# Optimization experiments

Measured on AMD Instinct MI355X. Metric: run time of the kernel, lower is better.

The kernel has to match this reference:

```python
import jax, jax.numpy as jnp
import numpy as np

B, S, HID = 1, 4096, 2048
NH, D = 16, 128
RATIO, TOPK, WIN = 4, 8, 128
ROPE_DIM = D // 2  # partial RoPE on first half of head_dim
EPS = 1e-6
NEG = -1e30


def rmsnorm(x, w):
    return x * jax.lax.rsqrt(jnp.mean(x * x, axis=-1, keepdims=True) + EPS) * w


def apply_rope(x, pos):
    # x: [..., L, D_head]; pos: [L] integer positions
    half = ROPE_DIM // 2
    inv = 1.0 / (10000.0 ** (jnp.arange(half, dtype=x.dtype) * (2.0 / ROPE_DIM)))
    ang = pos.astype(x.dtype)[:, None] * inv[None, :]  # [L, half]
    cos, sin = jnp.cos(ang), jnp.sin(ang)
    x1, x2, rest = x[..., :half], x[..., half:ROPE_DIM], x[..., ROPE_DIM:]
    return jnp.concatenate([x1 * cos - x2 * sin, x1 * sin + x2 * cos, rest], axis=-1)


def setup_inputs() -> dict:
    key = jax.random.key(0)
    ks = jax.random.split(key, 16)
    n = jax.random.normal
    s = 0.02
    return {
        "hidden_states": n(ks[0], (B, S, HID), jnp.float32),
        "Wq": n(ks[1], (HID, NH * D)) * s, "bq": jnp.zeros((NH * D,)),
        "Wcmp": n(ks[2], (HID, 1)) * s, "bcmp": jnp.zeros((1,)),
        "Wk": n(ks[3], (HID, D)) * s, "bk": jnp.zeros((D,)),
        "Wv": n(ks[4], (HID, D)) * s, "bv": jnp.zeros((D,)),
        "Wlk": n(ks[5], (HID, NH * D)) * s, "blk": jnp.zeros((NH * D,)),
        "Wlv": n(ks[6], (HID, NH * D)) * s, "blv": jnp.zeros((NH * D,)),
        "qn_w": jnp.ones((D,)), "kn_w": jnp.ones((D,)),
        "Wo": n(ks[7], (NH * D, HID)) * s, "bo": jnp.zeros((HID,)),
    }


def reference(hidden_states, Wq, bq, Wcmp, bcmp, Wk, bk, Wv, bv, Wlk, blk, Wlv, blv, qn_w, kn_w, Wo, bo):
    Bq, Sq, _ = hidden_states.shape
    C = Sq // RATIO
    scale = 1.0 / jnp.sqrt(jnp.float32(D))
    pos = jnp.arange(Sq)

    q = (hidden_states @ Wq + bq).reshape(Bq, Sq, NH, D).transpose(0, 2, 1, 3)  # [B,H,S,D]
    q = apply_rope(rmsnorm(q, qn_w), pos)

    # learned KV compression: softmax-weighted pooling within each block of size RATIO
    w_log = (hidden_states @ Wcmp + bcmp).reshape(Bq, C, RATIO)
    w_cmp = jax.nn.softmax(w_log, axis=-1)
    entries = jnp.einsum('bcr,bcrh->bch', w_cmp, hidden_states.reshape(Bq, C, RATIO, HID))
    block_ends = jnp.arange(1, C + 1) * RATIO - 1  # [C] last position of each block

    ck = apply_rope(rmsnorm(entries @ Wk + bk, kn_w), block_ends)  # [B,C,D] shared kv head
    cv = entries @ Wv + bv  # [B,C,D]

    # top-k block-sparse attention over compressed entries (causal on block_ends)
    sc = jnp.einsum('bhsd,bcd->bhsc', q, ck) * scale  # [B,H,S,C]
    causal = block_ends[None, None, None, :] <= pos[None, None, :, None]
    sc = jnp.where(causal, sc, NEG)
    tv, ti = jax.lax.top_k(sc, TOPK)  # [B,H,S,K]
    sel = (tv > NEG / 2).astype(sc.dtype)
    m = jnp.max(tv, axis=-1, keepdims=True)
    e = jnp.exp(tv - m) * sel
    pw = e / jnp.maximum(e.sum(axis=-1, keepdims=True), 1e-9)
    v_g = cv[jnp.arange(Bq)[:, None, None, None], ti]  # [B,H,S,K,D] irregular gather
    ctx_sparse = jnp.einsum('bhsk,bhskd->bhsd', pw, v_g)

    lk = apply_rope(rmsnorm((hidden_states @ Wlk + blk).reshape(Bq, Sq, NH, D).transpose(0, 2, 1, 3), kn_w), pos)
    lv = (hidden_states @ Wlv + blv).reshape(Bq, Sq, NH, D).transpose(0, 2, 1, 3)
    nc = Sq // WIN
    qc = q.reshape(Bq, NH, nc, WIN, D)

    def windowize(x):
        prev = jnp.pad(x, ((0, 0), (0, 0), (WIN, 0), (0, 0)))[:, :, :-WIN].reshape(Bq, NH, nc, WIN, D)
        cur = x.reshape(Bq, NH, nc, WIN, D)
        return jnp.concatenate([prev, cur], axis=3)  # [B,H,nc,2W,D]

    kw, vw = windowize(lk), windowize(lv)
    i = jnp.arange(WIN)[:, None]
    j = jnp.arange(2 * WIN)[None, :]
    rel = i + WIN - j  # qpos - kpos within the chunk pair
    band = (rel >= 0) & (rel <= WIN)
    kpos_ok = (jnp.arange(nc)[:, None, None] * WIN - WIN + j[None]) >= 0  # zero-pad chunk invalid
    mask = band[None] & kpos_ok  # [nc,W,2W]
    sl = jnp.einsum('bhcqd,bhckd->bhcqk', qc, kw) * scale
    sl = jnp.where(mask[None, None], sl, NEG)
    pl = jax.nn.softmax(sl, axis=-1)
    ctx_local = jnp.einsum('bhcqk,bhckd->bhcqd', pl, vw).reshape(Bq, NH, Sq, D)

    merged = (ctx_sparse + ctx_local) * 0.5  # mean over the two branches
    out = merged.transpose(0, 2, 1, 3).reshape(Bq, Sq, NH * D) @ Wo + bo
    return out
```

## Files before the change

kernel.cpp:

```cpp
#include <hip/hip_runtime.h>
#include <hip/hip_bf16.h>
#include <hip/hip_fp16.h>
#include <stdint.h>

typedef __hip_bfloat16 bf16;
using bf16x8 = __attribute__((ext_vector_type(8))) short;
using half8  = __attribute__((ext_vector_type(8))) _Float16;
using f32x4  = __attribute__((ext_vector_type(4))) float;

#define S_LEN   4096
#define HID_    2048
#define NH_     16
#define D_      128
#define C_      1024
#define SCALE_  0.08838834764831845f
#define DESC_   (1.0 / 1048576.0)

__device__ __forceinline__ float bflo(uint32_t u) {
  uint32_t x = (u & 0xffffu) << 16; float f; __builtin_memcpy(&f, &x, 4); return f;
}
__device__ __forceinline__ float bfhi(uint32_t u) {
  uint32_t x = u & 0xffff0000u; float f; __builtin_memcpy(&f, &x, 4); return f;
}
__device__ __forceinline__ void storeC(float* p, float v) { *p = v; }
__device__ __forceinline__ void storeC(bf16* p, float v)  { *p = __float2bfloat16(v); }
__device__ __forceinline__ void split2(float x, _Float16& h, _Float16& l) {
  h = (_Float16)x; l = (_Float16)(x - (float)h);
}
__device__ __forceinline__ short bf2s(bf16 b) { short s; __builtin_memcpy(&s, &b, 2); return s; }

__global__ __launch_bounds__(256) void cvt_k(const float* __restrict__ src, bf16* __restrict__ dst) {
  int i = (blockIdx.x * 256 + threadIdx.x) * 4;
  float4 v = *(const float4*)(src + i);
  bf16 o[4] = {__float2bfloat16(v.x), __float2bfloat16(v.y),
               __float2bfloat16(v.z), __float2bfloat16(v.w)};
  *(uint2*)(dst + i) = *(uint2*)o;
}

__global__ __launch_bounds__(256) void split_ck_k(const float* __restrict__ ckvF,
                                                  _Float16* __restrict__ oh, _Float16* __restrict__ ol) {
  int idx = blockIdx.x * 256 + threadIdx.x;
  int c = idx >> 7, k = idx & 127;
  float x = ckvF[(size_t)c * 256 + k] * 1024.0f;
  _Float16 h, l; split2(x, h, l);
  oh[idx] = h; ol[idx] = l;
}

__global__ __launch_bounds__(256) void transpose_k(const float* __restrict__ src,
                                                   bf16* __restrict__ dst, int R, int N) {
  __shared__ float tile[64][65];
  const int c0 = blockIdx.x * 64, r0 = blockIdx.y * 64;
  const int t = threadIdx.x, cc = t & 63, rb = t >> 6;
#pragma unroll
  for (int i = 0; i < 16; ++i) {
    int r = rb + i * 4;
    tile[r][cc] = src[(size_t)(r0 + r) * N + c0 + cc];
  }
  __syncthreads();
#pragma unroll
  for (int i = 0; i < 16; ++i) {
    int r = rb + i * 4;
    dst[(size_t)(c0 + r) * R + r0 + cc] = __float2bfloat16(tile[cc][r]);
  }
}

__global__ __launch_bounds__(256) void trans_f32s(const float* __restrict__ src,
                                                  float* __restrict__ dst, int R, int N) {
  __shared__ float tile[64][65];
  const int c0 = blockIdx.x * 64, r0 = blockIdx.y * 64;
  const int t = threadIdx.x, cc = t & 63, rb = t >> 6;
#pragma unroll
  for (int i = 0; i < 16; ++i) {
    int r = rb + i * 4;
    tile[r][cc] = src[(size_t)(r0 + r) * N + c0 + cc];
  }
  __syncthreads();
#pragma unroll
  for (int i = 0; i < 16; ++i) {
    int r = rb + i * 4;
    dst[(size_t)(c0 + r) * R + r0 + cc] = tile[cc][r] * 1024.0f;
  }
}

__global__ __launch_bounds__(256) void trans_v_k(const bf16* __restrict__ lklv, bf16* __restrict__ VT) {
  __shared__ ushort tile[64][65];
  const int s0 = blockIdx.x * 64, c0 = blockIdx.y * 64;
  const int t = threadIdx.x, cc = t & 63, rb = t >> 6;
  const ushort* src = (const ushort*)lklv;
#pragma unroll
  for (int i = 0; i < 16; ++i) {
    int r = rb + i * 4;
    tile[r][cc] = src[(size_t)(s0 + r) * 4096 + 2048 + c0 + cc];
  }
  __syncthreads();
  ushort* dst = (ushort*)VT;
#pragma unroll
  for (int i = 0; i < 16; ++i) {
    int r = rb + i * 4;
    dst[(size_t)(c0 + r) * 4096 + s0 + cc] = tile[cc][r];
  }
}

__global__ void build_bias(const float* bq, const float* blk, const float* blv,
                           const float* bk, const float* bv, const float* bo,
                           float* bQ, float* bLKLV, float* bKV, float* bO) {
  int i = blockIdx.x * 256 + threadIdx.x;
  if (i < 2048)       bQ[i] = bq[i];
  else if (i < 6144)  { int j = i - 2048; bLKLV[j] = (j < 2048) ? blk[j] : blv[j - 2048]; }
  else if (i < 6400)  { int j = i - 6144; bKV[j] = (j < 128) ? bk[j] : bv[j - 128]; }
  else if (i < 8448)  bO[i - 6400] = bo[i - 6400];
}

template <typename OutT>
__global__ __launch_bounds__(256) void gemm_bt(const bf16* __restrict__ A, const bf16* __restrict__ BT,
                                               const float* __restrict__ bias, OutT* __restrict__ Cmat,
                                               int M, int N, int K, int lda) {
  __shared__ bf16 As[128 * 32];
  __shared__ bf16 Bs[128 * 32];
  const int t = threadIdx.x;
  const int wave = t >> 6, lane = t & 63;
  const int wr = wave >> 1, wc = wave & 1;
  const int quad = lane >> 4, l15 = lane & 15;
  const int bx = blockIdx.x * 128, by = blockIdx.y * 128;
  const int srow = t >> 2, scol = (t & 3) * 8;
  f32x4 acc[4][4] = {};
  const bf16* a0 = A + (size_t)(by + srow) * lda + scol;
  const bf16* a1 = A + (size_t)(by + 64 + srow) * lda + scol;
  const bf16* b0 = BT + (size_t)(bx + srow) * K + scol;
  const bf16* b1 = BT + (size_t)(bx + 64 + srow) * K + scol;
  for (int k0 = 0; k0 < K; k0 += 32) {
    __builtin_amdgcn_global_load_lds((const __attribute__((address_space(1))) void*)(a0 + k0),
                                     (__attribute__((address_space(3))) void*)(As + t * 8), 16, 0, 0);
    __builtin_amdgcn_global_load_lds((const __attribute__((address_space(1))) void*)(a1 + k0),
                                     (__attribute__((address_space(3))) void*)(As + 2048 + t * 8), 16, 0, 0);
    __builtin_amdgcn_global_load_lds((const __attribute__((address_space(1))) void*)(b0 + k0),
                                     (__attribute__((address_space(3))) void*)(Bs + t * 8), 16, 0, 0);
    __builtin_amdgcn_global_load_lds((const __attribute__((address_space(1))) void*)(b1 + k0),
                                     (__attribute__((address_space(3))) void*)(Bs + 2048 + t * 8), 16, 0, 0);
    __syncthreads();
    bf16x8 aF[4], bF[4];
#pragma unroll
    for (int i = 0; i < 4; ++i)
      aF[i] = *(const bf16x8*)(As + (wr * 64 + i * 16 + l15) * 32 + quad * 8);
#pragma unroll
    for (int j = 0; j < 4; ++j)
      bF[j] = *(const bf16x8*)(Bs + (wc * 64 + j * 16 + l15) * 32 + quad * 8);
#pragma unroll
    for (int i = 0; i < 4; ++i)
#pragma unroll
      for (int j = 0; j < 4; ++j)
        acc[i][j] = __builtin_amdgcn_mfma_f32_16x16x32_bf16(aF[i], bF[j], acc[i][j], 0, 0, 0);
    __syncthreads();
  }
#pragma unroll
  for (int i = 0; i < 4; ++i)
#pragma unroll
    for (int j = 0; j < 4; ++j)
#pragma unroll
      for (int r = 0; r < 4; ++r) {
        int row = by + wr * 64 + i * 16 + quad * 4 + r;
        int col = bx + wc * 64 + j * 16 + l15;
        storeC(&Cmat[(size_t)row * N + col], acc[i][j][r] + bias[col]);
      }
}

__global__ __launch_bounds__(256) void gemm_prec4(const float* __restrict__ A, const float* __restrict__ BT,
                                                  const float* __restrict__ bias, float* __restrict__ Cmat,
                                                  int M, int N, int K, int lda) {
  __shared__ _Float16 Ah[128 * 32], Al[128 * 32], Bh[128 * 32], Bl[128 * 32];
  const int t = threadIdx.x;
  const int wave = t >> 6, lane = t & 63;
  const int wr = wave >> 1, wc = wave & 1;
  const int quad = lane >> 4, l15 = lane & 15;
  const int bx = blockIdx.x * 128, by = blockIdx.y * 128;
  double acc[4][4][4] = {};
  for (int k0 = 0; k0 < K; k0 += 32) {
#pragma unroll
    for (int it = 0; it < 4; ++it) {
      int sl = t + it * 256;
      int isB = sl >> 9, s2 = sl & 511, r = s2 >> 2, g = s2 & 3;
      const float* src = isB ? (BT + (size_t)(bx + r) * K + k0 + g * 8)
                             : (A  + (size_t)(by + r) * lda + k0 + g * 8);
      float4 u = ((const float4*)src)[0];
      float4 v = ((const float4*)src)[1];
      float xs[8] = {u.x, u.y, u.z, u.w, v.x, v.y, v.z, v.w};
      half8 hh, ll;
#pragma unroll
      for (int e = 0; e < 8; ++e) {
        float x = isB ? xs[e] : xs[e] * 1024.0f;
        _Float16 h, l; split2(x, h, l);
        hh[e] = h; ll[e] = l;
      }
      _Float16* dh = (isB ? Bh : Ah) + r * 32 + g * 8;
      _Float16* dl = (isB ? Bl : Al) + r * 32 + g * 8;
      *(half8*)dh = hh;
      *(half8*)dl = ll;
    }
    __syncthreads();
    half8 aFh[4], aFl[4], bFh[4], bFl[4];
#pragma unroll
    for (int i = 0; i < 4; ++i) {
      int ro = (wr * 64 + i * 16 + l15) * 32 + quad * 8;
      aFh[i] = *(const half8*)(Ah + ro);
      aFl[i] = *(const half8*)(Al + ro);
    }
#pragma unroll
    for (int j = 0; j < 4; ++j) {
      int ro = (wc * 64 + j * 16 + l15) * 32 + quad * 8;
      bFh[j] = *(const half8*)(Bh + ro);
      bFl[j] = *(const half8*)(Bl + ro);
    }
#pragma unroll
    for (int i = 0; i < 4; ++i)
#pragma unroll
      for (int j = 0; j < 4; ++j) {
        f32x4 tt = {0.f, 0.f, 0.f, 0.f};
        tt = __builtin_amdgcn_mfma_f32_16x16x32_f16(aFl[i], bFl[j], tt, 0, 0, 0);
        tt = __builtin_amdgcn_mfma_f32_16x16x32_f16(aFl[i], bFh[j], tt, 0, 0, 0);
        tt = __builtin_amdgcn_mfma_f32_16x16x32_f16(aFh[i], bFl[j], tt, 0, 0, 0);
        tt = __builtin_amdgcn_mfma_f32_16x16x32_f16(aFh[i], bFh[j], tt, 0, 0, 0);
#pragma unroll
        for (int r = 0; r < 4; ++r) acc[i][j][r] += (double)tt[r];
      }
    __syncthreads();
  }
#pragma unroll
  for (int i = 0; i < 4; ++i)
#pragma unroll
    for (int j = 0; j < 4; ++j)
#pragma unroll
      for (int r = 0; r < 4; ++r) {
        int row = by + wr * 64 + i * 16 + quad * 4 + r;
        int col = bx + wc * 64 + j * 16 + l15;
        Cmat[(size_t)row * N + col] = (float)(acc[i][j][r] * DESC_ + (double)bias[col]);
      }
}

__global__ __launch_bounds__(256) void normrope64(float* __restrict__ base, const float* __restrict__ w,
                                                  int nRows, int hPerS, int sStride,
                                                  int posMul, int posAdd) {
  int row = blockIdx.x * 4 + (threadIdx.x >> 6);
  int lane = threadIdx.x & 63;
  if (row >= nRows) return;
  int s = row / hPerS, h = row - s * hPerS;
  float* p = base + (size_t)s * sStride + h * 128;
  double x0 = (double)p[lane];
  double x1 = (double)p[lane + 64];
  double ss = x0 * x0 + x1 * x1;
#pragma unroll
  for (int m = 32; m; m >>= 1) ss += __shfl_xor(ss, m, 64);
  double rstd = 1.0 / sqrt(ss * (1.0 / 128.0) + 1e-6);
  double n0 = x0 * rstd * (double)w[lane];
  double n1 = x1 * rstd * (double)w[lane + 64];
  double other = __shfl_xor(n0, 32, 64);
  int fi = lane & 31;
  float invf = 1.0f / (float)pow(10000.0, (double)fi * (1.0 / 32.0));
  float angf = (float)(s * posMul + posAdd) * invf;
  double ang = (double)angf;
  double cs = cos(ang), sn = sin(ang);
  double r0 = (lane < 32) ? (n0 * cs - other * sn) : (other * sn + n0 * cs);
  p[lane] = (float)r0;
  p[lane + 64] = (float)n1;
}

__global__ __launch_bounds__(256) void normrope64_q(float* __restrict__ base, const float* __restrict__ w,
                                                    _Float16* __restrict__ qh, _Float16* __restrict__ ql) {
  __shared__ double csd[32], snd[32];
  const int s = blockIdx.x;
  const int t = threadIdx.x, wv = t >> 6, lane = t & 63;
  if (t < 32) {
    float invf = 1.0f / (float)pow(10000.0, (double)t * (1.0 / 32.0));
    float angf = (float)s * invf;
    double ang = (double)angf;
    csd[t] = cos(ang);
    snd[t] = sin(ang);
  }
  __syncthreads();
  const int fi = lane & 31;
  float* ps = base + (size_t)s * HID_;
  for (int h = wv; h < 16; h += 4) {
    float* p = ps + h * 128;
    double x0 = (double)p[lane];
    double x1 = (double)p[lane + 64];
    double ss = x0 * x0 + x1 * x1;
#pragma unroll
    for (int m = 32; m; m >>= 1) ss += __shfl_xor(ss, m, 64);
    double rstd = 1.0 / sqrt(ss * (1.0 / 128.0) + 1e-6);
    double n0 = x0 * rstd * (double)w[lane];
    double n1 = x1 * rstd * (double)w[lane + 64];
    double other = __shfl_xor(n0, 32, 64);
    double cs = csd[fi], sn = snd[fi];
    double r0 = (lane < 32) ? (n0 * cs - other * sn) : (other * sn + n0 * cs);
    float f0 = (float)r0, f1 = (float)n1;
    p[lane] = f0;
    p[lane + 64] = f1;
    _Float16 h0, l0, h1, l1;
    split2(f0 * 1024.0f, h0, l0);
    split2(f1 * 1024.0f, h1, l1);
    size_t off = (size_t)s * HID_ + h * 128;
    qh[off + lane] = h0;       ql[off + lane] = l0;
    qh[off + 64 + lane] = h1;  ql[off + 64 + lane] = l1;
  }
}

__global__ __launch_bounds__(256) void normrope_bf_l(bf16* __restrict__ base, const float* __restrict__ w) {
  __shared__ float csf[32], snf[32];
  const int s = blockIdx.x;
  const int t = threadIdx.x, wv = t >> 6, lane = t & 63;
  if (t < 32) {
    float invf = 1.0f / (float)pow(10000.0, (double)t * (1.0 / 32.0));
    float ang = (float)s * invf;
    csf[t] = cosf(ang);
    snf[t] = sinf(ang);
  }
  __syncthreads();
  const int fi = lane & 31;
  bf16* ps = base + (size_t)s * 4096;
  for (int h = wv; h < 16; h += 4) {
    bf16* p = ps + h * 128;
    float x0 = __bfloat162float(p[lane]);
    float x1 = __bfloat162float(p[lane + 64]);
    float ss = x0 * x0 + x1 * x1;
#pragma unroll
    for (int m = 32; m; m >>= 1) ss += __shfl_xor(ss, m, 64);
    float rstd = rsqrtf(ss * 0.0078125f + 1e-6f);
    float n0 = x0 * rstd * w[lane];
    float n1 = x1 * rstd * w[lane + 64];
    float other = __shfl_xor(n0, 32, 64);
    float cs = csf[fi], sn = snf[fi];
    float r0 = (lane < 32) ? (n0 * cs - other * sn) : (other * sn + n0 * cs);
    p[lane] = __float2bfloat16(r0);
    p[lane + 64] = __float2bfloat16(n1);
  }
}

__global__ __launch_bounds__(256) void wlog_k(const float* __restrict__ hidden, const float* __restrict__ wcmp,
                                              const float* __restrict__ bcmp, float* __restrict__ wlog) {
  int s = blockIdx.x * 4 + (threadIdx.x >> 6);
  int lane = threadIdx.x & 63;
  const float* hp = hidden + (size_t)s * HID_;
  double acc = 0.0;
  for (int i = lane; i < HID_; i += 64)
    acc += (double)hp[i] * (double)wcmp[i];
#pragma unroll
  for (int m = 32; m; m >>= 1) acc += __shfl_xor(acc, m, 64);
  if (lane == 0) wlog[s] = (float)(acc + (double)bcmp[0]);
}

__global__ void wsm_k(const float* __restrict__ wlog, float* __restrict__ wsm) {
  int c = blockIdx.x * 256 + threadIdx.x;
  if (c >= C_) return;
  double v[4], m = -1e300;
#pragma unroll
  for (int r = 0; r < 4; ++r) { v[r] = (double)wlog[4 * c + r]; if (v[r] > m) m = v[r]; }
  double sum = 0.0;
#pragma unroll
  for (int r = 0; r < 4; ++r) { v[r] = exp(v[r] - m); sum += v[r]; }
#pragma unroll
  for (int r = 0; r < 4; ++r) wsm[4 * c + r] = (float)(v[r] / sum);
}

__global__ __launch_bounds__(256) void entries_k(const float* __restrict__ hidden, const float* __restrict__ wsm,
                                                 float* __restrict__ entriesF) {
  int idx = blockIdx.x * 256 + threadIdx.x;
  int c = idx >> 11, hcol = idx & 2047;
  double e = 0.0;
#pragma unroll
  for (int r = 0; r < 4; ++r)
    e += (double)wsm[4 * c + r] * (double)hidden[(size_t)(4 * c + r) * HID_ + hcol];
  entriesF[idx] = (float)e;
}

__global__ __launch_bounds__(1024, 8) void sparse_v9(const _Float16* __restrict__ qh, const _Float16* __restrict__ ql,
                                                     const _Float16* __restrict__ ckh, const _Float16* __restrict__ ckl,
                                                     const float* __restrict__ ckvF, bf16* __restrict__ sp) {
  __shared__ float sc[16 * 1024];
  const int by = blockIdx.y;
  const int s0 = blockIdx.x * 8;
  const int t = threadIdx.x, w = t >> 6, lane = t & 63;
  const int quad = lane >> 4, l15 = lane & 15;
  const int nvmax  = (s0 >> 2) + 2;
  const int ntiles = (nvmax + 15) >> 4;
  const double esc = (double)SCALE_ * DESC_;

  if (w < ntiles) {
    const int sA = s0 + (l15 & 7);
    const int hA = 2 * by + (l15 >> 3);
    half8 aFh[4], aFl[4];
    {
      const _Float16* qbh = qh + (size_t)sA * HID_ + hA * 128 + quad * 8;
      const _Float16* qbl = ql + (size_t)sA * HID_ + hA * 128 + quad * 8;
#pragma unroll
      for (int kk = 0; kk < 4; ++kk) {
        aFh[kk] = *(const half8*)(qbh + kk * 32);
        aFl[kk] = *(const half8*)(qbl + kk * 32);
      }
    }
    for (int ct = w; ct < ntiles; ct += 16) {
      const int c0 = ct * 16;
      const _Float16* kbh = ckh + (size_t)(c0 + l15) * 128 + quad * 8;
      const _Float16* kbl = ckl + (size_t)(c0 + l15) * 128 + quad * 8;
      double a64[4] = {0.0, 0.0, 0.0, 0.0};
#pragma unroll
      for (int kk = 0; kk < 4; ++kk) {
        half8 bh = *(const half8*)(kbh + kk * 32);
        half8 bl = *(const half8*)(kbl + kk * 32);
        f32x4 tt = {0.f, 0.f, 0.f, 0.f};
        tt = __builtin_amdgcn_mfma_f32_16x16x32_f16(aFl[kk], bl, tt, 0, 0, 0);
        tt = __builtin_amdgcn_mfma_f32_16x16x32_f16(aFl[kk], bh, tt, 0, 0, 0);
        tt = __builtin_amdgcn_mfma_f32_16x16x32_f16(aFh[kk], bl, tt, 0, 0, 0);
        tt = __builtin_amdgcn_mfma_f32_16x16x32_f16(aFh[kk], bh, tt, 0, 0, 0);
#pragma unroll
        for (int r = 0; r < 4; ++r) a64[r] += (double)tt[r];
      }
#pragma unroll
      for (int r = 0; r < 4; ++r)
        sc[(quad * 4 + r) * 1024 + c0 + l15] = (float)(a64[r] * esc);
    }
  }
  __syncthreads();
  if (w >= 4) return;

  const int q = w * 4 + quad;
  const int p2 = q >> 3, wq = q & 7;
  const int s = s0 + wq;
  const int nv = (s >= 3) ? (((s - 3) >> 2) + 1) : 0;
  const float* srow = sc + q * 1024;
  const int jmaxB = (nvmax + 63) >> 6;

  float tv0 = -1e38f, tv1 = -1e38f, tv2 = -1e38f, tv3 = -1e38f;
  int   ti0 = 0x40000000, ti1 = 0x40000000, ti2 = 0x40000000, ti3 = 0x40000000;
  for (int j = 0; j < jmaxB; ++j) {
    int cb = j * 64 + l15 * 4;
    float4 vv = *(const float4*)(srow + cb);
    float xs[4] = {vv.x, vv.y, vv.z, vv.w};
#pragma unroll
    for (int e = 0; e < 4; ++e) {
      int c = cb + e;
      float v = (c < nv) ? xs[e] : -1e38f;
      if (v > tv3) {
        if (v > tv0)      { tv3=tv2;ti3=ti2; tv2=tv1;ti2=ti1; tv1=tv0;ti1=ti0; tv0=v;ti0=c; }
        else if (v > tv1) { tv3=tv2;ti3=ti2; tv2=tv1;ti2=ti1; tv1=v;ti1=c; }
        else if (v > tv2) { tv3=tv2;ti3=ti2; tv2=v;ti2=c; }
        else              { tv3=v;ti3=c; }
      }
    }
  }

  unsigned long long deadm = 0ull;
  int ncons = 0;
  float bvs[8]; int bis[8];
#pragma unroll
  for (int it = 0; it < 8; ++it) {
    float bv = tv0; int bi = ti0;
#pragma unroll
    for (int mm = 1; mm <= 8; mm <<= 1) {
      float ov = __shfl_xor(bv, mm, 64);
      int   oi = __shfl_xor(bi, mm, 64);
      if (ov > bv || (ov == bv && oi < bi)) { bv = ov; bi = oi; }
    }
    bvs[it] = bv; bis[it] = bi;
    if (bv > -1e29f && (((bi >> 2) & 15) == l15)) {
      deadm |= 1ull << (((bi >> 6) << 2) | (bi & 3));
      tv0=tv1;ti0=ti1; tv1=tv2;ti1=ti2; tv2=tv3;ti2=ti3;
      tv3=-1e38f; ti3=0x40000000;
      if (++ncons == 4) {
        ncons = 0;
        tv0=tv1=tv2=tv3=-1e38f;
        ti0=ti1=ti2=ti3=0x40000000;
        for (int j = 0; j < jmaxB; ++j) {
          int cb = j * 64 + l15 * 4;
          float4 vv = *(const float4*)(srow + cb);
          float xs[4] = {vv.x, vv.y, vv.z, vv.w};
#pragma unroll
          for (int e = 0; e < 4; ++e) {
            int c = cb + e;
            int li = ((c >> 6) << 2) | (c & 3);
            float v = (c < nv && !((deadm >> li) & 1ull)) ? xs[e] : -1e38f;
            if (v > tv3) {
              if (v > tv0)      { tv3=tv2;ti3=ti2; tv2=tv1;ti2=ti1; tv1=tv0;ti1=ti0; tv0=v;ti0=c; }
              else if (v > tv1) { tv3=tv2;ti3=ti2; tv2=tv1;ti2=ti1; tv1=v;ti1=c; }
              else if (v > tv2) { tv3=tv2;ti3=ti2; tv2=v;ti2=c; }
              else              { tv3=v;ti3=c; }
            }
          }
        }
      }
    }
  }

  const float m0 = bvs[0];
  float a0=0.f,a1=0.f,a2=0.f,a3=0.f,a4=0.f,a5=0.f,a6=0.f,a7=0.f;
  float esum = 0.f;
#pragma unroll
  for (int it = 0; it < 8; ++it) {
    if (bvs[it] > -1e29f) {
      float wgt = expf(bvs[it] - m0);
      esum += wgt;
      const float* cvp = ckvF + (size_t)bis[it] * 256 + 128 + l15 * 8;
      float4 u = *(const float4*)cvp;
      float4 v = *(const float4*)(cvp + 4);
      a0 += wgt*u.x; a1 += wgt*u.y; a2 += wgt*u.z; a3 += wgt*u.w;
      a4 += wgt*v.x; a5 += wgt*v.y; a6 += wgt*v.z; a7 += wgt*v.w;
    }
  }
  float inv = 1.0f / fmaxf(esum, 1e-9f);
  bf16* op = sp + (size_t)s * 2048 + (2 * by + p2) * 128 + l15 * 8;
  bf16 ob[8] = {__float2bfloat16(a0*inv), __float2bfloat16(a1*inv),
                __float2bfloat16(a2*inv), __float2bfloat16(a3*inv),
                __float2bfloat16(a4*inv), __float2bfloat16(a5*inv),
                __float2bfloat16(a6*inv), __float2bfloat16(a7*inv)};
  *(uint4*)op = *(uint4*)ob;
}

__global__ __launch_bounds__(128) void local_mfma(const float* __restrict__ qf,
                                                  const bf16* __restrict__ lklv,
                                                  const bf16* __restrict__ VT,
                                                  const bf16* __restrict__ sp,
                                                  bf16* __restrict__ merged) {
  constexpr int PADP = 168;
  __shared__ bf16 PhS[2][16 * PADP];
  __shared__ bf16 PlS[2][16 * PADP];
  const int h = blockIdx.y;
  const int t = threadIdx.x, w = t >> 6, lane = t & 63;
  const int quad = lane >> 4, l15 = lane & 15;
  const int sw = blockIdx.x * 32 + w * 16;
  const int kbase = sw - 128;
  const int ridx = quad * 4;

  bf16x8 qH[4], qL[4];
  {
    const float* qp = qf + (size_t)(sw + l15) * HID_ + h * 128 + quad * 8;
#pragma unroll
    for (int kk = 0; kk < 4; ++kk) {
      float4 u = *(const float4*)(qp + kk * 32);
      float4 v = *(const float4*)(qp + kk * 32 + 4);
      float xs[8] = {u.x, u.y, u.z, u.w, v.x, v.y, v.z, v.w};
      bf16x8 hh, ll;
#pragma unroll
      for (int e = 0; e < 8; ++e) {
        bf16 bh = __float2bfloat16(xs[e]);
        float fh = __bfloat162float(bh);
        bf16 bl = __float2bfloat16(xs[e] - fh);
        hh[e] = bf2s(bh); ll[e] = bf2s(bl);
      }
      qH[kk] = hh; qL[kk] = ll;
    }
  }

  float sc[9][4];
#pragma unroll
  for (int ct = 0; ct < 9; ++ct) {
    int key0 = kbase + ct * 16 + l15;
    const bf16* kp = lklv + (size_t)(key0 < 0 ? 0 : key0) * 4096 + h * 128 + quad * 8;
    f32x4 acc = {0.f, 0.f, 0.f, 0.f};
#pragma unroll
    for (int kk = 0; kk < 4; ++kk) {
      bf16x8 kb = *(const bf16x8*)(kp + kk * 32);
      acc = __builtin_amdgcn_mfma_f32_16x16x32_bf16(qL[kk], kb, acc, 0, 0, 0);
      acc = __builtin_amdgcn_mfma_f32_16x16x32_bf16(qH[kk], kb, acc, 0, 0, 0);
    }
// ... 23 lines not shown
  for (int z = lane; z < 256; z += 64) {
    int zr = z >> 4, zc = z & 15;
    phb[zr * PADP + 144 + zc] = __float2bfloat16(0.f);
    plb[zr * PADP + 144 + zc] = __float2bfloat16(0.f);
  }
  float lsum[4] = {0.f, 0.f, 0.f, 0.f};
#pragma unroll
  for (int ct = 0; ct < 9; ++ct) {
    int cidx = ct * 16 + l15;
#pragma unroll
    for (int r = 0; r < 4; ++r) {
      float e = (sc[ct][r] > -1e29f) ? expf(sc[ct][r] - mrow[r]) : 0.f;
      lsum[r] += e;
      bf16 bh = __float2bfloat16(e);
      float fh = __bfloat162float(bh);
      bf16 bl = __float2bfloat16(e - fh);
      phb[(ridx + r) * PADP + cidx] = bh;
      plb[(ridx + r) * PADP + cidx] = bl;
    }
  }
#pragma unroll
  for (int mm = 1; mm <= 8; mm <<= 1)
#pragma unroll
    for (int r = 0; r < 4; ++r) lsum[r] += __shfl_xor(lsum[r], mm, 64);
  float inv[4];
#pragma unroll
  for (int r = 0; r < 4; ++r) inv[r] = 1.0f / lsum[r];

  bf16x8 pH[5], pL[5];
#pragma unroll
  for (int kk = 0; kk < 5; ++kk) {
    pH[kk] = *(const bf16x8*)(phb + l15 * PADP + kk * 32 + quad * 8);
    pL[kk] = *(const bf16x8*)(plb + l15 * PADP + kk * 32 + quad * 8);
  }

#pragma unroll
  for (int dt = 0; dt < 8; ++dt) {
    const bf16* vrow = VT + (size_t)(h * 128 + dt * 16 + l15) * 4096;
    f32x4 acc = {0.f, 0.f, 0.f, 0.f};
#pragma unroll
    for (int kk = 0; kk < 5; ++kk) {
      int ko = kbase + kk * 32 + quad * 8;
      ko = ko < 0 ? 0 : (ko > 4088 ? 4088 : ko);
      bf16x8 vb = *(const bf16x8*)(vrow + ko);
      acc = __builtin_amdgcn_mfma_f32_16x16x32_bf16(pL[kk], vb, acc, 0, 0, 0);
      acc = __builtin_amdgcn_mfma_f32_16x16x32_bf16(pH[kk], vb, acc, 0, 0, 0);
    }
#pragma unroll
    for (int r = 0; r < 4; ++r) {
      int srow = sw + ridx + r;
      size_t off = (size_t)srow * 2048 + h * 128 + dt * 16 + l15;
      float spv = __bfloat162float(sp[off]);
      merged[off] = __float2bfloat16((acc[r] * inv[r] + spv) * 0.5f);
    }
  }
}

extern "C" void kernel_launch(void* const* d_in, const int* in_sizes, int n_in,
                              void* d_out, int out_size, void* d_ws, size_t ws_size,
                              hipStream_t stream) {
  (void)in_sizes; (void)n_in; (void)out_size; (void)ws_size;
  const float* hidden = (const float*)d_in[0];
  const float* Wq   = (const float*)d_in[1];
  const float* bq   = (const float*)d_in[2];
  const float* Wcmp = (const float*)d_in[3];
  const float* bcmp = (const float*)d_in[4];
  const float* Wk   = (const float*)d_in[5];
  const float* bk   = (const float*)d_in[6];
  const float* Wv   = (const float*)d_in[7];
  const float* bv   = (const float*)d_in[8];
  const float* Wlk  = (const float*)d_in[9];
  const float* blk  = (const float*)d_in[10];
  const float* Wlv  = (const float*)d_in[11];
  const float* blv  = (const float*)d_in[12];
  const float* qn_w = (const float*)d_in[13];
  const float* kn_w = (const float*)d_in[14];
  const float* Wo   = (const float*)d_in[15];
  const float* bo   = (const float*)d_in[16];
  float* out = (float*)d_out;

  char* ws = (char*)d_ws;
  float*    qf       = (float*)   (ws);
  bf16*     lklv     = (bf16*)    (ws + 33554432);
  float*    WqTs     = (float*)   (ws + 67108864);
  _Float16* qh       = (_Float16*)(ws + 67108864);
  bf16*     VT       = (bf16*)    (ws + 67108864);
  bf16*     hbf      = (bf16*)    (ws + 83886080);
  bf16*     merged   = (bf16*)    (ws + 83886080);
  bf16*     bt_lklv  = (bf16*)    (ws + 100663296);
  bf16*     sp       = (bf16*)    (ws + 100663296);
  float*    WkvTs    = (float*)   (ws + 117440512);
  bf16*     WoT      = (bf16*)    (ws + 119537664);
  float*    entriesF = (float*)   (ws + 127926272);
  float*    ckvF     = (float*)   (ws + 136314880);
  _Float16* ckh      = (_Float16*)(ws + 137363456);
  _Float16* ckl      = (_Float16*)(ws + 137625600);
  float*    wlog     = (float*)   (ws + 137887744);
  float*    wsm      = (float*)   (ws + 137904128);
  float*    bQ       = (float*)   (ws + 137920512);
  float*    bLKLV    = (float*)   (ws + 137928704);
  float*    bKV      = (float*)   (ws + 137945088);
  float*    bO       = (float*)   (ws + 137946112);
  _Float16* ql       = (_Float16*)(ws + 137954304);

  cvt_k<<<dim3(8192), dim3(256), 0, stream>>>(hidden, hbf);

  trans_f32s<<<dim3(32, 32), dim3(256), 0, stream>>>(Wq, WqTs, HID_, HID_);
  trans_f32s<<<dim3(2, 32),  dim3(256), 0, stream>>>(Wk, WkvTs, HID_, 128);
  trans_f32s<<<dim3(2, 32),  dim3(256), 0, stream>>>(Wv, WkvTs + (size_t)128 * HID_, HID_, 128);
  transpose_k<<<dim3(32, 32), dim3(256), 0, stream>>>(Wlk, bt_lklv, HID_, HID_);
  transpose_k<<<dim3(32, 32), dim3(256), 0, stream>>>(Wlv, bt_lklv + (size_t)2048 * HID_, HID_, HID_);
  transpose_k<<<dim3(32, 32), dim3(256), 0, stream>>>(Wo, WoT, HID_, HID_);
  build_bias<<<dim3(33), dim3(256), 0, stream>>>(bq, blk, blv, bk, bv, bo, bQ, bLKLV, bKV, bO);

  wlog_k<<<dim3(1024), dim3(256), 0, stream>>>(hidden, Wcmp, bcmp, wlog);
  wsm_k<<<dim3(4), dim3(256), 0, stream>>>(wlog, wsm);
  entries_k<<<dim3(8192), dim3(256), 0, stream>>>(hidden, wsm, entriesF);

  gemm_prec4<<<dim3(16, 32), dim3(256), 0, stream>>>(hidden,   WqTs,  bQ,  qf,   S_LEN, HID_, HID_, HID_);
  gemm_prec4<<<dim3(2, 8),   dim3(256), 0, stream>>>(entriesF, WkvTs, bKV, ckvF, C_,    256,  HID_, HID_);
  gemm_bt<bf16><<<dim3(32, 32), dim3(256), 0, stream>>>(hbf, bt_lklv, bLKLV, lklv, S_LEN, 4096, HID_, HID_);

  normrope64_q<<<dim3(4096), dim3(256), 0, stream>>>(qf, qn_w, qh, ql);
  normrope64<<<dim3(256),   dim3(256), 0, stream>>>(ckvF, kn_w, 1024, 1, 256, 4, 3);
  normrope_bf_l<<<dim3(4096), dim3(256), 0, stream>>>(lklv, kn_w);

  split_ck_k<<<dim3(512), dim3(256), 0, stream>>>(ckvF, ckh, ckl);

  sparse_v9<<<dim3(512, 8), dim3(1024), 0, stream>>>(qh, ql, ckh, ckl, ckvF, sp);
  trans_v_k<<<dim3(64, 32), dim3(256), 0, stream>>>(lklv, VT);
  local_mfma<<<dim3(128, 16), dim3(128), 0, stream>>>(qf, lklv, VT, sp, merged);

  gemm_bt<float><<<dim3(16, 32), dim3(256), 0, stream>>>(merged, WoT, bO, out, S_LEN, HID_, HID_, HID_);
}
```

Before: 1.108 ms.

## Fuse setup kernels, pre-split Q GEMM operands, and unroll sparse score tiles

Folds the bias build into the bf16 conversion kernel. Merges the three bf16 weight transposes and the two Wk/Wv transposes into single launches, and fuses the ck hi/lo split into the normrope kernel. The Q projection now pre-splits hidden and Wq into fp16 hi/lo arrays once and runs a new GEMM on them, so the split is no longer done inside the tiles. The sparse kernel scores two key tiles per loop iteration and uses a strided top-k scan layout. Together these cut launch count and in-kernel conversion work, at the cost of extra workspace traffic for the split arrays and more register pressure in the sparse kernel.

```diff
diff --git a/kernel.cpp b/kernel.cpp
--- a/kernel.cpp
+++ b/kernel.cpp
@@ -16,12 +16,6 @@
 #define SCALE_  0.08838834764831845f
 #define DESC_   (1.0 / 1048576.0)
 
-__device__ __forceinline__ float bflo(uint32_t u) {
-  uint32_t x = (u & 0xffffu) << 16; float f; __builtin_memcpy(&f, &x, 4); return f;
-}
-__device__ __forceinline__ float bfhi(uint32_t u) {
-  uint32_t x = u & 0xffff0000u; float f; __builtin_memcpy(&f, &x, 4); return f;
-}
 __device__ __forceinline__ void storeC(float* p, float v) { *p = v; }
 __device__ __forceinline__ void storeC(bf16* p, float v)  { *p = __float2bfloat16(v); }
 __device__ __forceinline__ void split2(float x, _Float16& h, _Float16& l) {
@@ -29,56 +23,100 @@
 }
 __device__ __forceinline__ short bf2s(bf16 b) { short s; __builtin_memcpy(&s, &b, 2); return s; }
 
-__global__ __launch_bounds__(256) void cvt_k(const float* __restrict__ src, bf16* __restrict__ dst) {
+#define GLDS(src, dst) __builtin_amdgcn_global_load_lds( \
+    (const __attribute__((address_space(1))) void*)(src), \
+    (__attribute__((address_space(3))) void*)(dst), 16, 0, 0)
+
+__global__ __launch_bounds__(256) void cvt_bias_k(const float* __restrict__ src, bf16* __restrict__ dst,
+                                                  const float* bq, const float* blk, const float* blv,
+                                                  const float* bk, const float* bv, const float* bo,
+                                                  float* bQ, float* bLKLV, float* bKV, float* bO) {
   int i = (blockIdx.x * 256 + threadIdx.x) * 4;
   float4 v = *(const float4*)(src + i);
   bf16 o[4] = {__float2bfloat16(v.x), __float2bfloat16(v.y),
                __float2bfloat16(v.z), __float2bfloat16(v.w)};
   *(uint2*)(dst + i) = *(uint2*)o;
-}
-
-__global__ __launch_bounds__(256) void split_ck_k(const float* __restrict__ ckvF,
-                                                  _Float16* __restrict__ oh, _Float16* __restrict__ ol) {
-  int idx = blockIdx.x * 256 + threadIdx.x;
-  int c = idx >> 7, k = idx & 127;
-  float x = ckvF[(size_t)c * 256 + k] * 1024.0f;
-  _Float16 h, l; split2(x, h, l);
-  oh[idx] = h; ol[idx] = l;
-}
-
-__global__ __launch_bounds__(256) void transpose_k(const float* __restrict__ src,
-                                                   bf16* __restrict__ dst, int R, int N) {
+  int ib = blockIdx.x * 256 + threadIdx.x;
+  if (ib < 8448) {
+    if (ib < 2048)      bQ[ib] = bq[ib];
+    else if (ib < 6144) { int j = ib - 2048; bLKLV[j] = (j < 2048) ? blk[j] : blv[j - 2048]; }
+    else if (ib < 6400) { int j = ib - 6144; bKV[j] = (j < 128) ? bk[j] : bv[j - 128]; }
+    else                bO[ib - 6400] = bo[ib - 6400];
+  }
+}
+
+__global__ __launch_bounds__(256) void split_q_k(const float* __restrict__ src,
+                                                 _Float16* __restrict__ oh, _Float16* __restrict__ ol) {
+  int i = (blockIdx.x * 256 + threadIdx.x) * 4;
+  float4 v = *(const float4*)(src + i);
+  float xs[4] = {v.x, v.y, v.z, v.w};
+  _Float16 hh[4], ll[4];
+#pragma unroll
+  for (int e = 0; e < 4; ++e) split2(xs[e] * 1024.0f, hh[e], ll[e]);
+  *(uint2*)(oh + i) = *(uint2*)hh;
+  *(uint2*)(ol + i) = *(uint2*)ll;
+}
+
+__global__ __launch_bounds__(256) void trans_split_wq(const float* __restrict__ src,
+                                                      _Float16* __restrict__ oh, _Float16* __restrict__ ol) {
   __shared__ float tile[64][65];
   const int c0 = blockIdx.x * 64, r0 = blockIdx.y * 64;
   const int t = threadIdx.x, cc = t & 63, rb = t >> 6;
 #pragma unroll
   for (int i = 0; i < 16; ++i) {
     int r = rb + i * 4;
-    tile[r][cc] = src[(size_t)(r0 + r) * N + c0 + cc];
+    tile[r][cc] = src[(size_t)(r0 + r) * HID_ + c0 + cc];
   }
   __syncthreads();
 #pragma unroll
   for (int i = 0; i < 16; ++i) {
     int r = rb + i * 4;
-    dst[(size_t)(c0 + r) * R + r0 + cc] = __float2bfloat16(tile[cc][r]);
-  }
-}
-
-__global__ __launch_bounds__(256) void trans_f32s(const float* __restrict__ src,
-                                                  float* __restrict__ dst, int R, int N) {
+    float x = tile[cc][r] * 1024.0f;
+    _Float16 h, l; split2(x, h, l);
+    size_t off = (size_t)(c0 + r) * HID_ + r0 + cc;
+    oh[off] = h; ol[off] = l;
+  }
+}
+
+__global__ __launch_bounds__(256) void transpose3_k(const float* __restrict__ Wlk, const float* __restrict__ Wlv,
+                                                    const float* __restrict__ Wo,
+                                                    bf16* __restrict__ bt_lklv, bf16* __restrict__ WoT) {
   __shared__ float tile[64][65];
+  const float* src = (blockIdx.z == 0) ? Wlk : (blockIdx.z == 1) ? Wlv : Wo;
+  bf16* dst = (blockIdx.z == 0) ? bt_lklv
+            : (blockIdx.z == 1) ? (bt_lklv + (size_t)2048 * HID_) : WoT;
   const int c0 = blockIdx.x * 64, r0 = blockIdx.y * 64;
   const int t = threadIdx.x, cc = t & 63, rb = t >> 6;
 #pragma unroll
   for (int i = 0; i < 16; ++i) {
     int r = rb + i * 4;
-    tile[r][cc] = src[(size_t)(r0 + r) * N + c0 + cc];
+    tile[r][cc] = src[(size_t)(r0 + r) * HID_ + c0 + cc];
   }
   __syncthreads();
 #pragma unroll
   for (int i = 0; i < 16; ++i) {
     int r = rb + i * 4;
-    dst[(size_t)(c0 + r) * R + r0 + cc] = tile[cc][r] * 1024.0f;
+    dst[(size_t)(c0 + r) * HID_ + r0 + cc] = __float2bfloat16(tile[cc][r]);
+  }
+}
+
+__global__ __launch_bounds__(256) void trans_f32s_kv(const float* __restrict__ Wk, const float* __restrict__ Wv,
+                                                     float* __restrict__ WkvTs) {
+  __shared__ float tile[64][65];
+  const float* src = blockIdx.z ? Wv : Wk;
+  float* dst = WkvTs + (blockIdx.z ? (size_t)128 * HID_ : 0);
+  const int c0 = blockIdx.x * 64, r0 = blockIdx.y * 64;
+  const int t = threadIdx.x, cc = t & 63, rb = t >> 6;
+#pragma unroll
+  for (int i = 0; i < 16; ++i) {
+    int r = rb + i * 4;
+    tile[r][cc] = src[(size_t)(r0 + r) * 128 + c0 + cc];
+  }
+  __syncthreads();
+#pragma unroll
+  for (int i = 0; i < 16; ++i) {
+    int r = rb + i * 4;
+    dst[(size_t)(c0 + r) * HID_ + r0 + cc] = tile[cc][r] * 1024.0f;
   }
 }
 
@@ -99,16 +137,6 @@
     int r = rb + i * 4;
     dst[(size_t)(c0 + r) * 4096 + s0 + cc] = tile[cc][r];
   }
-}
-
-__global__ void build_bias(const float* bq, const float* blk, const float* blv,
-                           const float* bk, const float* bv, const float* bo,
-                           float* bQ, float* bLKLV, float* bKV, float* bO) {
-  int i = blockIdx.x * 256 + threadIdx.x;
-  if (i < 2048)       bQ[i] = bq[i];
-  else if (i < 6144)  { int j = i - 2048; bLKLV[j] = (j < 2048) ? blk[j] : blv[j - 2048]; }
-  else if (i < 6400)  { int j = i - 6144; bKV[j] = (j < 128) ? bk[j] : bv[j - 128]; }
-  else if (i < 8448)  bO[i - 6400] = bo[i - 6400];
 }
 
 template <typename OutT>
@@ -129,14 +157,10 @@
   const bf16* b0 = BT + (size_t)(bx + srow) * K + scol;
   const bf16* b1 = BT + (size_t)(bx + 64 + srow) * K + scol;
   for (int k0 = 0; k0 < K; k0 += 32) {
-    __builtin_amdgcn_global_load_lds((const __attribute__((address_space(1))) void*)(a0 + k0),
-                                     (__attribute__((address_space(3))) void*)(As + t * 8), 16, 0, 0);
-    __builtin_amdgcn_global_load_lds((const __attribute__((address_space(1))) void*)(a1 + k0),
-                                     (__attribute__((address_space(3))) void*)(As + 2048 + t * 8), 16, 0, 0);
-    __builtin_amdgcn_global_load_lds((const __attribute__((address_space(1))) void*)(b0 + k0),
-                                     (__attribute__((address_space(3))) void*)(Bs + t * 8), 16, 0, 0);
-    __builtin_amdgcn_global_load_lds((const __attribute__((address_space(1))) void*)(b1 + k0),
-                                     (__attribute__((address_space(3))) void*)(Bs + 2048 + t * 8), 16, 0, 0);
+    GLDS(a0 + k0, As + t * 8);
+    GLDS(a1 + k0, As + 2048 + t * 8);
+    GLDS(b0 + k0, Bs + t * 8);
+    GLDS(b1 + k0, Bs + 2048 + t * 8);
     __syncthreads();
     bf16x8 aF[4], bF[4];
 #pragma unroll
@@ -161,6 +185,75 @@
         int row = by + wr * 64 + i * 16 + quad * 4 + r;
         int col = bx + wc * 64 + j * 16 + l15;
         storeC(&Cmat[(size_t)row * N + col], acc[i][j][r] + bias[col]);
+      }
+}
+
+__global__ __launch_bounds__(256) void gemm_hl4(const _Float16* __restrict__ Ah, const _Float16* __restrict__ Al,
+                                                const _Float16* __restrict__ Bh, const _Float16* __restrict__ Bl,
+                                                const float* __restrict__ bias, float* __restrict__ Cmat,
+                                                int M, int N, int K, int lda) {
+  __shared__ _Float16 Ahs[128 * 32], Als[128 * 32], Bhs[128 * 32], Bls[128 * 32];
+  const int t = threadIdx.x;
+  const int wave = t >> 6, lane = t & 63;
+  const int wr = wave >> 1, wc = wave & 1;
+  const int quad = lane >> 4, l15 = lane & 15;
+  const int bx = blockIdx.x * 128, by = blockIdx.y * 128;
+  const int srow = t >> 2, scol = (t & 3) * 8;
+  double acc[4][4][4] = {};
+  const _Float16* a0h = Ah + (size_t)(by + srow) * lda + scol;
+  const _Float16* a1h = Ah + (size_t)(by + 64 + srow) * lda + scol;
+  const _Float16* a0l = Al + (size_t)(by + srow) * lda + scol;
+  const _Float16* a1l = Al + (size_t)(by + 64 + srow) * lda + scol;
+  const _Float16* b0h = Bh + (size_t)(bx + srow) * K + scol;
+  const _Float16* b1h = Bh + (size_t)(bx + 64 + srow) * K + scol;
+  const _Float16* b0l = Bl + (size_t)(bx + srow) * K + scol;
+  const _Float16* b1l = Bl + (size_t)(bx + 64 + srow) * K + scol;
+  for (int k0 = 0; k0 < K; k0 += 32) {
+    GLDS(a0h + k0, Ahs + t * 8);
+    GLDS(a1h + k0, Ahs + 2048 + t * 8);
+    GLDS(a0l + k0, Als + t * 8);
+    GLDS(a1l + k0, Als + 2048 + t * 8);
+    GLDS(b0h + k0, Bhs + t * 8);
+    GLDS(b1h + k0, Bhs + 2048 + t * 8);
+    GLDS(b0l + k0, Bls + t * 8);
+    GLDS(b1l + k0, Bls + 2048 + t * 8);
+    __syncthreads();
+    half8 aFh[4], aFl[4], bFh[4], bFl[4];
+#pragma unroll
+    for (int i = 0; i < 4; ++i) {
+      int ro = (wr * 64 + i * 16 + l15) * 32 + quad * 8;
+      aFh[i] = *(const half8*)(Ahs + ro);
+      aFl[i] = *(const half8*)(Als + ro);
+    }
+#pragma unroll
+    for (int j = 0; j < 4; ++j) {
+      int ro = (wc * 64 + j * 16 + l15) * 32 + quad * 8;
+      bFh[j] = *(const half8*)(Bhs + ro);
+      bFl[j] = *(const half8*)(Bls + ro);
+    }
+#pragma unroll
+    for (int i = 0; i < 4; ++i)
+#pragma unroll
+      for (int j = 0; j < 4; ++j) {
+        f32x4 tt = {0.f, 0.f, 0.f, 0.f};
+        tt = __builtin_amdgcn_mfma_f32_16x16x32_f16(aFl[i], bFl[j], tt, 0, 0, 0);
+        tt = __builtin_amdgcn_mfma_f32_16x16x32_f16(aFl[i], bFh[j], tt, 0, 0, 0);
+        tt = __builtin_amdgcn_mfma_f32_16x16x32_f16(aFh[i], bFl[j], tt, 0, 0, 0);
+        tt = __builtin_amdgcn_mfma_f32_16x16x32_f16(aFh[i], bFh[j], tt, 0, 0, 0);
+#pragma unroll
+        for (int r = 0; r < 4; ++r) acc[i][j][r] += (double)tt[r];
+      }
+    __syncthreads();
+  }
+#pragma unroll
+  for (int i = 0; i < 4; ++i)
+#pragma unroll
+    for (int j = 0; j < 4; ++j)
+#pragma unroll
+      for (int r = 0; r < 4; ++r) {
+        int row = by + wr * 64 + i * 16 + quad * 4 + r;
+        int col = bx + wc * 64 + j * 16 + l15;
+        Cmat[(size_t)row * N + col] = (float)(acc[i][j][r] * DESC_ + (double)bias[col]);
       }
 }
 
@@ -234,33 +327,6 @@
         int col = bx + wc * 64 + j * 16 + l15;
         Cmat[(size_t)row * N + col] = (float)(acc[i][j][r] * DESC_ + (double)bias[col]);
       }
-}
-
-__global__ __launch_bounds__(256) void normrope64(float* __restrict__ base, const float* __restrict__ w,
-                                                  int nRows, int hPerS, int sStride,
-                                                  int posMul, int posAdd) {
-  int row = blockIdx.x * 4 + (threadIdx.x >> 6);
-  int lane = threadIdx.x & 63;
-  if (row >= nRows) return;
-  int s = row / hPerS, h = row - s * hPerS;
-  float* p = base + (size_t)s * sStride + h * 128;
-  double x0 = (double)p[lane];
-  double x1 = (double)p[lane + 64];
-  double ss = x0 * x0 + x1 * x1;
-#pragma unroll
-  for (int m = 32; m; m >>= 1) ss += __shfl_xor(ss, m, 64);
-  double rstd = 1.0 / sqrt(ss * (1.0 / 128.0) + 1e-6);
-  double n0 = x0 * rstd * (double)w[lane];
-  double n1 = x1 * rstd * (double)w[lane + 64];
-  double other = __shfl_xor(n0, 32, 64);
-  int fi = lane & 31;
-  float invf = 1.0f / (float)pow(10000.0, (double)fi * (1.0 / 32.0));
-  float angf = (float)(s * posMul + posAdd) * invf;
-  double ang = (double)angf;
-  double cs = cos(ang), sn = sin(ang);
-  double r0 = (lane < 32) ? (n0 * cs - other * sn) : (other * sn + n0 * cs);
-  p[lane] = (float)r0;
-  p[lane + 64] = (float)n1;
 }
 
 __global__ __launch_bounds__(256) void normrope64_q(float* __restrict__ base, const float* __restrict__ w,
@@ -303,6 +369,36 @@
   }
 }
 
+__global__ __launch_bounds__(256) void normrope64_ck(float* __restrict__ base, const float* __restrict__ w,
+                                                     _Float16* __restrict__ ckh, _Float16* __restrict__ ckl) {
+  int row = blockIdx.x * 4 + (threadIdx.x >> 6);
+  int lane = threadIdx.x & 63;
+  float* p = base + (size_t)row * 256;
+  double x0 = (double)p[lane];
+  double x1 = (double)p[lane + 64];
+  double ss = x0 * x0 + x1 * x1;
+#pragma unroll
+  for (int m = 32; m; m >>= 1) ss += __shfl_xor(ss, m, 64);
+  double rstd = 1.0 / sqrt(ss * (1.0 / 128.0) + 1e-6);
+  double n0 = x0 * rstd * (double)w[lane];
+  double n1 = x1 * rstd * (double)w[lane + 64];
+  double other = __shfl_xor(n0, 32, 64);
+  int fi = lane & 31;
+  float invf = 1.0f / (float)pow(10000.0, (double)fi * (1.0 / 32.0));
+  float angf = (float)(row * 4 + 3) * invf;
+  double ang = (double)angf;
+  double cs = cos(ang), sn = sin(ang);
+  double r0 = (lane < 32) ? (n0 * cs - other * sn) : (other * sn + n0 * cs);
+  float f0 = (float)r0, f1 = (float)n1;
+  p[lane] = f0;
+  p[lane + 64] = f1;
+  _Float16 h0, l0, h1, l1;
+  split2(f0 * 1024.0f, h0, l0);
+  split2(f1 * 1024.0f, h1, l1);
+  ckh[row * 128 + lane] = h0;       ckl[row * 128 + lane] = l0;
+  ckh[row * 128 + 64 + lane] = h1;  ckl[row * 128 + 64 + lane] = l1;
+}
+
 __global__ __launch_bounds__(256) void normrope_bf_l(bf16* __restrict__ base, const float* __restrict__ w) {
   __shared__ float csf[32], snf[32];
   const int s = blockIdx.x;
@@ -371,9 +467,9 @@
   entriesF[idx] = (float)e;
 }
 
-__global__ __launch_bounds__(1024, 8) void sparse_v9(const _Float16* __restrict__ qh, const _Float16* __restrict__ ql,
-                                                     const _Float16* __restrict__ ckh, const _Float16* __restrict__ ckl,
-                                                     const float* __restrict__ ckvF, bf16* __restrict__ sp) {
+__global__ __launch_bounds__(1024, 8) void sparse_v10(const _Float16* __restrict__ qh, const _Float16* __restrict__ ql,
+                                                      const _Float16* __restrict__ ckh, const _Float16* __restrict__ ckl,
+                                                      const float* __restrict__ ckvF, bf16* __restrict__ sp) {
   __shared__ float sc[16 * 1024];
   const int by = blockIdx.y;
   const int s0 = blockIdx.x * 8;
@@ -396,26 +492,43 @@
         aFl[kk] = *(const half8*)(qbl + kk * 32);
       }
     }
-    for (int ct = w; ct < ntiles; ct += 16) {
-      const int c0 = ct * 16;
-      const _Float16* kbh = ckh + (size_t)(c0 + l15) * 128 + quad * 8;
-      const _Float16* kbl = ckl + (size_t)(c0 + l15) * 128 + quad * 8;
-      double a64[4] = {0.0, 0.0, 0.0, 0.0};
+    for (int ct = w; ct < ntiles; ct += 32) {
+      const int c0a = ct * 16;
+      const bool two = (ct + 16) < ntiles;
+      const int c0b = two ? (ct + 16) * 16 : c0a;
+      const _Float16* kbha = ckh + (size_t)(c0a + l15) * 128 + quad * 8;
+      const _Float16* kbla = ckl + (size_t)(c0a + l15) * 128 + quad * 8;
+      const _Float16* kbhb = ckh + (size_t)(c0b + l15) * 128 + quad * 8;
+      const _Float16* kblb = ckl + (size_t)(c0b + l15) * 128 + quad * 8;
+      double a64a[4] = {0.0, 0.0, 0.0, 0.0};
+      double a64b[4] = {0.0, 0.0, 0.0, 0.0};
 #pragma unroll
       for (int kk = 0; kk < 4; ++kk) {
-        half8 bh = *(const half8*)(kbh + kk * 32);
-        half8 bl = *(const half8*)(kbl + kk * 32);
-        f32x4 tt = {0.f, 0.f, 0.f, 0.f};
-        tt = __builtin_amdgcn_mfma_f32_16x16x32_f16(aFl[kk], bl, tt, 0, 0, 0);
-        tt = __builtin_amdgcn_mfma_f32_16x16x32_f16(aFl[kk], bh, tt, 0, 0, 0);
-        tt = __builtin_amdgcn_mfma_f32_16x16x32_f16(aFh[kk], bl, tt, 0, 0, 0);
-        tt = __builtin_amdgcn_mfma_f32_16x16x32_f16(aFh[kk], bh, tt, 0, 0, 0);
-#pragma unroll
-        for (int r = 0; r < 4; ++r) a64[r] += (double)tt[r];
+        half8 bha = *(const half8*)(kbha + kk * 32);
+        half8 bla = *(const half8*)(kbla + kk * 32);
+        half8 bhb = *(const half8*)(kbhb + kk * 32);
+        half8 blb = *(const half8*)(kblb + kk * 32);
+        f32x4 tta = {0.f, 0.f, 0.f, 0.f};
+        tta = __builtin_amdgcn_mfma_f32_16x16x32_f16(aFl[kk], bla, tta, 0, 0, 0);
+        tta = __builtin_amdgcn_mfma_f32_16x16x32_f16(aFl[kk], bha, tta, 0, 0, 0);
+        tta = __builtin_amdgcn_mfma_f32_16x16x32_f16(aFh[kk], bla, tta, 0, 0, 0);
+        tta = __builtin_amdgcn_mfma_f32_16x16x32_f16(aFh[kk], bha, tta, 0, 0, 0);
+        f32x4 ttb = {0.f, 0.f, 0.f, 0.f};
+        ttb = __builtin_amdgcn_mfma_f32_16x16x32_f16(aFl[kk], blb, ttb, 0, 0, 0);
+        ttb = __builtin_amdgcn_mfma_f32_16x16x32_f16(aFl[kk], bhb, ttb, 0, 0, 0);
+        ttb = __builtin_amdgcn_mfma_f32_16x16x32_f16(aFh[kk], blb, ttb, 0, 0, 0);
+        ttb = __builtin_amdgcn_mfma_f32_16x16x32_f16(aFh[kk], bhb, ttb, 0, 0, 0);
+#pragma unroll
+        for (int r = 0; r < 4; ++r) { a64a[r] += (double)tta[r]; a64b[r] += (double)ttb[r]; }
       }
 #pragma unroll
       for (int r = 0; r < 4; ++r)
-        sc[(quad * 4 + r) * 1024 + c0 + l15] = (float)(a64[r] * esc);
+        sc[(quad * 4 + r) * 1024 + c0a + l15] = (float)(a64a[r] * esc);
+      if (two) {
+#pragma unroll
+        for (int r = 0; r < 4; ++r)
+          sc[(quad * 4 + r) * 1024 + c0b + l15] = (float)(a64b[r] * esc);
+      }
     }
   }
   __syncthreads();
@@ -425,19 +538,17 @@
   const int p2 = q >> 3, wq = q & 7;
   const int s = s0 + wq;
   const int nv = (s >= 3) ? (((s - 3) >> 2) + 1) : 0;
-  const float* srow = sc + q * 1024;
+  const float* srowL = sc + q * 1024 + l15;
   const int jmaxB = (nvmax + 63) >> 6;
 
   float tv0 = -1e38f, tv1 = -1e38f, tv2 = -1e38f, tv3 = -1e38f;
   int   ti0 = 0x40000000, ti1 = 0x40000000, ti2 = 0x40000000, ti3 = 0x40000000;
   for (int j = 0; j < jmaxB; ++j) {
-    int cb = j * 64 + l15 * 4;
-    float4 vv = *(const float4*)(srow + cb);
-    float xs[4] = {vv.x, vv.y, vv.z, vv.w};
+    int base = j * 64;
 #pragma unroll
     for (int e = 0; e < 4; ++e) {
-      int c = cb + e;
-      float v = (c < nv) ? xs[e] : -1e38f;
+      int c = base + e * 16 + l15;
+      float v = (c < nv) ? srowL[base + e * 16] : -1e38f;
       if (v > tv3) {
         if (v > tv0)      { tv3=tv2;ti3=ti2; tv2=tv1;ti2=ti1; tv1=tv0;ti1=ti0; tv0=v;ti0=c; }
         else if (v > tv1) { tv3=tv2;ti3=ti2; tv2=tv1;ti2=ti1; tv1=v;ti1=c; }
@@ -460,8 +571,8 @@
       if (ov > bv || (ov == bv && oi < bi)) { bv = ov; bi = oi; }
     }
     bvs[it] = bv; bis[it] = bi;
-    if (bv > -1e29f && (((bi >> 2) & 15) == l15)) {
-      deadm |= 1ull << (((bi >> 6) << 2) | (bi & 3));
+    if (bv > -1e29f && ((bi & 15) == l15)) {
+      deadm |= 1ull << (((bi >> 6) << 2) | ((bi >> 4) & 3));
       tv0=tv1;ti0=ti1; tv1=tv2;ti1=ti2; tv2=tv3;ti2=ti3;
       tv3=-1e38f; ti3=0x40000000;
       if (++ncons == 4) {
@@ -469,14 +580,12 @@
         tv0=tv1=tv2=tv3=-1e38f;
         ti0=ti1=ti2=ti3=0x40000000;
         for (int j = 0; j < jmaxB; ++j) {
-          int cb = j * 64 + l15 * 4;
-          float4 vv = *(const float4*)(srow + cb);
-          float xs[4] = {vv.x, vv.y, vv.z, vv.w};
+          int base = j * 64;
 #pragma unroll
           for (int e = 0; e < 4; ++e) {
-            int c = cb + e;
-            int li = ((c >> 6) << 2) | (c & 3);
-            float v = (c < nv && !((deadm >> li) & 1ull)) ? xs[e] : -1e38f;
+            int c = base + e * 16 + l15;
+            int li = (j << 2) | e;
+            float v = (c < nv && !((deadm >> li) & 1ull)) ? srowL[base + e * 16] : -1e38f;
             if (v > tv3) {
               if (v > tv0)      { tv3=tv2;ti3=ti2; tv2=tv1;ti2=ti1; tv1=tv0;ti1=ti0; tv0=v;ti0=c; }
               else if (v > tv1) { tv3=tv2;ti3=ti2; tv2=tv1;ti2=ti1; tv1=v;ti1=c; }
@@ -666,12 +775,13 @@
   char* ws = (char*)d_ws;
   float*    qf       = (float*)   (ws);
   bf16*     lklv     = (bf16*)    (ws + 33554432);
-  float*    WqTs     = (float*)   (ws + 67108864);
   _Float16* qh       = (_Float16*)(ws + 67108864);
   bf16*     VT       = (bf16*)    (ws + 67108864);
   bf16*     hbf      = (bf16*)    (ws + 83886080);
+  _Float16* hidh     = (_Float16*)(ws + 83886080);
   bf16*     merged   = (bf16*)    (ws + 83886080);
   bf16*     bt_lklv  = (bf16*)    (ws + 100663296);
+  _Float16* hidl     = (_Float16*)(ws + 100663296);
   bf16*     sp       = (bf16*)    (ws + 100663296);
   float*    WkvTs    = (float*)   (ws + 117440512);
   bf16*     WoT      = (bf16*)    (ws + 119537664);
@@ -685,33 +795,31 @@
   float*    bLKLV    = (float*)   (ws + 137928704);
   float*    bKV      = (float*)   (ws + 137945088);
   float*    bO       = (float*)   (ws + 137946112);
+  _Float16* wqh      = (_Float16*)(ws + 137954304);
+  _Float16* wql      = (_Float16*)(ws + 146342912);
   _Float16* ql       = (_Float16*)(ws + 137954304);
 
-  cvt_k<<<dim3(8192), dim3(256), 0, stream>>>(hidden, hbf);
-
-  trans_f32s<<<dim3(32, 32), dim3(256), 0, stream>>>(Wq, WqTs, HID_, HID_);
-  trans_f32s<<<dim3(2, 32),  dim3(256), 0, stream>>>(Wk, WkvTs, HID_, 128);
-  trans_f32s<<<dim3(2, 32),  dim3(256), 0, stream>>>(Wv, WkvTs + (size_t)128 * HID_, HID_, 128);
-  transpose_k<<<dim3(32, 32), dim3(256), 0, stream>>>(Wlk, bt_lklv, HID_, HID_);
-  transpose_k<<<dim3(32, 32), dim3(256), 0, stream>>>(Wlv, bt_lklv + (size_t)2048 * HID_, HID_, HID_);
-  transpose_k<<<dim3(32, 32), dim3(256), 0, stream>>>(Wo, WoT, HID_, HID_);
-  build_bias<<<dim3(33), dim3(256), 0, stream>>>(bq, blk, blv, bk, bv, bo, bQ, bLKLV, bKV, bO);
+  cvt_bias_k<<<dim3(8192), dim3(256), 0, stream>>>(hidden, hbf, bq, blk, blv, bk, bv, bo,
+                                                   bQ, bLKLV, bKV, bO);
+  transpose3_k<<<dim3(32, 32, 3), dim3(256), 0, stream>>>(Wlk, Wlv, Wo, bt_lklv, WoT);
+  trans_f32s_kv<<<dim3(2, 32, 2), dim3(256), 0, stream>>>(Wk, Wv, WkvTs);
 
   wlog_k<<<dim3(1024), dim3(256), 0, stream>>>(hidden, Wcmp, bcmp, wlog);
   wsm_k<<<dim3(4), dim3(256), 0, stream>>>(wlog, wsm);
   entries_k<<<dim3(8192), dim3(256), 0, stream>>>(hidden, wsm, entriesF);
 
-  gemm_prec4<<<dim3(16, 32), dim3(256), 0, stream>>>(hidden,   WqTs,  bQ,  qf,   S_LEN, HID_, HID_, HID_);
-  gemm_prec4<<<dim3(2, 8),   dim3(256), 0, stream>>>(entriesF, WkvTs, bKV, ckvF, C_,    256,  HID_, HID_);
   gemm_bt<bf16><<<dim3(32, 32), dim3(256), 0, stream>>>(hbf, bt_lklv, bLKLV, lklv, S_LEN, 4096, HID_, HID_);
+  gemm_prec4<<<dim3(2, 8), dim3(256), 0, stream>>>(entriesF, WkvTs, bKV, ckvF, C_, 256, HID_, HID_);
+
+  split_q_k<<<dim3(8192), dim3(256), 0, stream>>>(hidden, hidh, hidl);
+  trans_split_wq<<<dim3(32, 32), dim3(256), 0, stream>>>(Wq, wqh, wql);
+  gemm_hl4<<<dim3(16, 32), dim3(256), 0, stream>>>(hidh, hidl, wqh, wql, bQ, qf, S_LEN, HID_, HID_, HID_);
 
   normrope64_q<<<dim3(4096), dim3(256), 0, stream>>>(qf, qn_w, qh, ql);
-  normrope64<<<dim3(256),   dim3(256), 0, stream>>>(ckvF, kn_w, 1024, 1, 256, 4, 3);
+  normrope64_ck<<<dim3(256), dim3(256), 0, stream>>>(ckvF, kn_w, ckh, ckl);
   normrope_bf_l<<<dim3(4096), dim3(256), 0, stream>>>(lklv, kn_w);
 
-  split_ck_k<<<dim3(512), dim3(256), 0, stream>>>(ckvF, ckh, ckl);
-
-  sparse_v9<<<dim3(512, 8), dim3(1024), 0, stream>>>(qh, ql, ckh, ckl, ckvF, sp);
+  sparse_v10<<<dim3(512, 8), dim3(1024), 0, stream>>>(qh, ql, ckh, ckl, ckvF, sp);
   trans_v_k<<<dim3(64, 32), dim3(256), 0, stream>>>(lklv, VT);
   local_mfma<<<dim3(128, 16), dim3(128), 0, stream>>>(qf, lklv, VT, sp, merged);
 
```

New measurement: 1.220 ms. 1.1x slower.
